# Optimization experiments

Hardware: AMD Instinct MI355X
Metric: run time of the kernel (lower is better)

## Reference

```python
import jax, jax.numpy as jnp
import numpy as np

EMBED_DIM = 768
N_HEADS = 12
HEAD_DIM = EMBED_DIM // N_HEADS


def setup_inputs() -> dict:
    key = jax.random.key(0)
    ks = jax.random.split(key, 6)
    bsz, seq = 2, 4096
    hidden_states = jax.random.normal(ks[0], (bsz, seq, EMBED_DIM), dtype=jnp.float32)
    attention_mask = jnp.zeros((bsz, 1, 1, seq), dtype=jnp.float32)
    s = 1.0 / np.sqrt(EMBED_DIM)
    Wq = jax.random.normal(ks[1], (EMBED_DIM, EMBED_DIM), dtype=jnp.float32) * s
    Wk = jax.random.normal(ks[2], (EMBED_DIM, EMBED_DIM), dtype=jnp.float32) * s
    Wv = jax.random.normal(ks[3], (EMBED_DIM, EMBED_DIM), dtype=jnp.float32) * s
    Wo = jax.random.normal(ks[4], (EMBED_DIM, EMBED_DIM), dtype=jnp.float32) * s
    bo = jax.random.normal(ks[5], (EMBED_DIM,), dtype=jnp.float32) * s
    return {"hidden_states": hidden_states, "attention_mask": attention_mask,
            "Wq": Wq, "Wk": Wk, "Wv": Wv, "Wo": Wo, "bo": bo}


def reference(hidden_states, attention_mask, Wq, Wk, Wv, Wo, bo):
    bsz, seq, _ = hidden_states.shape
    scale = 1.0 / np.sqrt(HEAD_DIM)

    def split_heads(x):  # [b, s, e] -> [b, h, s, d]
        return x.reshape(bsz, seq, N_HEADS, HEAD_DIM).transpose(0, 2, 1, 3)

    # nn.Linear applies x @ W.T
    q = split_heads(hidden_states @ Wq.T)
    k = split_heads(hidden_states @ Wk.T)
    v = split_heads(hidden_states @ Wv.T)

    # [b, h, tgt, src] score matrix (faithful to the bmm+softmax+bmm original)
    attn = jnp.einsum('bhqd,bhkd->bhqk', q, k) * scale
    attn = attn + attention_mask  # mask broadcasts [b,1,1,src]
    probs = jax.nn.softmax(attn, axis=-1)
    ctx = jnp.einsum('bhqk,bhkd->bhqd', probs, v)

    concat = ctx.transpose(0, 2, 1, 3).reshape(bsz, seq, EMBED_DIM)
    return concat @ Wo.T + bo
```

## Files before the change

kernel.cpp:

```cpp
#include <hip/hip_runtime.h>
#include <stdint.h>

#define ED   768
#define NH   12
#define HD   64
#define SEQ  4096
#define BSZ  2
#define BHT  (BSZ*NH)
#define MTOT (BSZ*SEQ)

typedef short bf16x8  __attribute__((ext_vector_type(8)));
typedef float f32x4   __attribute__((ext_vector_type(4)));
typedef float f32x16  __attribute__((ext_vector_type(16)));

#define LOG2E 1.44269504088896340736f
#define C2    (0.125f * LOG2E)

__device__ __forceinline__ unsigned short f2bf(float f) {
    union { float f; uint32_t u; } v; v.f = f;
    uint32_t u = v.u;
    u += 0x7fffu + ((u >> 16) & 1u);
    return (unsigned short)(u >> 16);
}

__device__ __forceinline__ void cp16(const unsigned short* g, unsigned short* l) {
    __builtin_amdgcn_global_load_lds(
        (const __attribute__((address_space(1))) unsigned int*)(const void*)g,
        (__attribute__((address_space(3))) unsigned int*)(void*)l,
        16, 0, 0);
}

#define H_CHUNKS  (MTOT * ED / 4)
#define W_CHUNKS  (ED * ED / 4)
#define CVT_TOTAL (H_CHUNKS + 4 * W_CHUNKS)

__global__ __launch_bounds__(256) void convert_bf16(
    const float* __restrict__ H,  const float* __restrict__ Wq,
    const float* __restrict__ Wk, const float* __restrict__ Wv,
    const float* __restrict__ Wo, unsigned short* __restrict__ dst,
    unsigned short* __restrict__ WoB) {
    int i4 = blockIdx.x * 256 + threadIdx.x;
    float4 v;
    ushort4* optr;
    if (i4 < H_CHUNKS) { v = ((const float4*)H)[i4]; optr = (ushort4*)dst + i4; }
    else {
        int j = i4 - H_CHUNKS;
        if (j < 3 * W_CHUNKS) {
            if (j < W_CHUNKS)          v = ((const float4*)Wq)[j];
            else if (j < 2 * W_CHUNKS) v = ((const float4*)Wk)[j - W_CHUNKS];
            else                       v = ((const float4*)Wv)[j - 2 * W_CHUNKS];
            optr = (ushort4*)dst + i4;
        } else {
            v = ((const float4*)Wo)[j - 3 * W_CHUNKS];
            optr = (ushort4*)WoB + (j - 3 * W_CHUNKS);
        }
    }
    ushort4 o;
    o.x = f2bf(v.x); o.y = f2bf(v.y); o.z = f2bf(v.z); o.w = f2bf(v.w);
    *optr = o;
}

__global__ __launch_bounds__(256) void qkv_gemm(
    const unsigned short* __restrict__ Hb,
    const unsigned short* __restrict__ Wb,
    unsigned short* __restrict__ qkv) {
    __shared__ __align__(16) unsigned short Ah[128 * 64];
    __shared__ __align__(16) unsigned short Bh[128 * 64];
    const int t = threadIdx.x, w = t >> 6, lane = t & 63;
    const int quad = lane >> 4, r16 = lane & 15;
    const int wm = w >> 1, wn = w & 1;
    const int m0 = blockIdx.y * 128, n0g = blockIdx.x * 128;
    const int wsel = n0g / ED, n0 = n0g % ED;
    const int lrow = lane >> 3;
    const int lchs = ((lane & 7) ^ (lrow & 7)) * 8;

    f32x4 acc[4][4] = {};
    for (int kt = 0; kt < ED / 64; ++kt) {
        const int k0 = kt * 64;
#pragma unroll
        for (int i = 0; i < 4; ++i) {
            int row = i * 32 + w * 8;
            cp16(&Hb[(size_t)(m0 + row + lrow) * ED + k0 + lchs], &Ah[row * 64]);
            cp16(&Wb[(size_t)(n0g + row + lrow) * ED + k0 + lchs], &Bh[row * 64]);
        }
        __syncthreads();
#pragma unroll
        for (int kk = 0; kk < 2; ++kk) {
            bf16x8 aF[4], bF[4];
#pragma unroll
            for (int mi = 0; mi < 4; ++mi) {
                int R = wm * 64 + mi * 16 + r16;
                aF[mi] = *(const bf16x8*)&Ah[R * 64 + (((kk * 4 + quad) ^ (r16 & 7)) * 8)];
            }
#pragma unroll
            for (int ni = 0; ni < 4; ++ni) {
                int R = wn * 64 + ni * 16 + r16;
                bF[ni] = *(const bf16x8*)&Bh[R * 64 + (((kk * 4 + quad) ^ (r16 & 7)) * 8)];
            }
            if (wsel == 2) {
#pragma unroll
                for (int mi = 0; mi < 4; ++mi)
#pragma unroll
                    for (int ni = 0; ni < 4; ++ni)
                        acc[mi][ni] = __builtin_amdgcn_mfma_f32_16x16x32_bf16(
                            bF[ni], aF[mi], acc[mi][ni], 0, 0, 0);
            } else {
#pragma unroll
                for (int mi = 0; mi < 4; ++mi)
#pragma unroll
                    for (int ni = 0; ni < 4; ++ni)
                        acc[mi][ni] = __builtin_amdgcn_mfma_f32_16x16x32_bf16(
                            aF[mi], bF[ni], acc[mi][ni], 0, 0, 0);
            }
        }
        __syncthreads();
    }
    const size_t WSZ = (size_t)BHT * SEQ * HD;
    if (wsel == 2) {
#pragma unroll
        for (int mi = 0; mi < 4; ++mi)
#pragma unroll
            for (int ni = 0; ni < 4; ++ni)
#pragma unroll
                for (int r = 0; r < 4; ++r) {
                    int m  = m0 + wm * 64 + mi * 16 + r16;
                    int nn = n0 + wn * 64 + ni * 16 + quad * 4 + r;
                    int b = m >> 12, s = m & 4095;
                    int hh = nn >> 6, dd = nn & 63;
                    qkv[2 * WSZ + (((size_t)b * NH + hh) * HD + dd) * SEQ + s] =
                        f2bf(acc[mi][ni][r]);
                }
    } else {
        const float sc = (wsel == 0) ? C2 : 1.0f;
#pragma unroll
        for (int mi = 0; mi < 4; ++mi)
#pragma unroll
            for (int ni = 0; ni < 4; ++ni)
#pragma unroll
                for (int r = 0; r < 4; ++r) {
                    int m = m0 + wm * 64 + mi * 16 + quad * 4 + r;
                    int b = m >> 12, s = m & 4095;
                    int nn = n0 + wn * 64 + ni * 16 + r16;
                    int hh = nn >> 6, dd = nn & 63;
                    size_t off = (((size_t)b * NH + hh) * SEQ + s) * HD + dd;
                    qkv[(size_t)wsel * WSZ + off] = f2bf(acc[mi][ni][r] * sc);
                }
    }
}

__global__ __launch_bounds__(256) void flash_attn(
    const unsigned short* __restrict__ qkv, const float* __restrict__ mask,
    unsigned short* __restrict__ ctx) {
    __shared__ __align__(16) unsigned short Ksm[64 * 64];
    __shared__ __align__(16) unsigned short Vtsm[64 * 64];
    __shared__ __align__(16) unsigned short Psm[4][32][72];
    __shared__ unsigned short Msm[64];
    const int t  = threadIdx.x;
    const int bh = blockIdx.y;
    const int b  = bh / NH;
    const int h  = bh % NH;
    const int qbase = blockIdx.x * 128;
    const size_t WSZ = (size_t)BHT * SEQ * HD;
    const unsigned short* Qp = qkv + (size_t)bh * SEQ * HD;
    const unsigned short* Kp = Qp + WSZ;
    const unsigned short* Vt = qkv + 2 * WSZ + (size_t)bh * HD * SEQ;
    const int w = t >> 6, lane = t & 63, n31 = lane & 31, hi = lane >> 5;
    const int lrow = lane >> 3;
    const int lchs = ((lane & 7) ^ (lrow & 7)) * 8;

    bf16x8 qF[4];
    {
        int qrow = qbase + w * 32 + n31;
#pragma unroll
        for (int kc = 0; kc < 4; ++kc)
            qF[kc] = *(const bf16x8*)&Qp[(size_t)qrow * HD + kc * 16 + hi * 8];
    }
    bf16x8 bOnes = {};
    if (hi == 0) bOnes[0] = (short)0x3F80;

    f32x16 oAcc[2] = {};
    float l_i = 0.0f;
    const int sw = n31 & 7;

    for (int kt = 0; kt < SEQ / 64; ++kt) {
#pragma unroll
        for (int i = 0; i < 2; ++i) {
            int row = w * 16 + i * 8;
            cp16(&Kp[(size_t)(kt * 64 + row + lrow) * HD + lchs], &Ksm[row * 64]);
            cp16(&Vt[(size_t)(row + lrow) * SEQ + kt * 64 + lchs], &Vtsm[row * 64]);
        }
        if (t < 64) Msm[t] = f2bf(LOG2E * mask[b * SEQ + kt * 64 + t]);
        __syncthreads();

        float p[2][16];
        float rs0 = 0.f, rs1 = 0.f, rs2 = 0.f, rs3 = 0.f;
#pragma unroll
        for (int st = 0; st < 2; ++st) {
            bf16x8 am = {};
            {
                unsigned short mv = Msm[st * 32 + n31];
                am[0] = (hi == 0) ? (short)mv : (short)0;
            }
            f32x16 sA = {};
            sA = __builtin_amdgcn_mfma_f32_32x32x16_bf16(am, bOnes, sA, 0, 0, 0);
#pragma unroll
            for (int kc = 0; kc < 4; ++kc) {
                bf16x8 kF = *(const bf16x8*)
                    &Ksm[(st * 32 + n31) * 64 + (((2 * kc + hi) ^ sw) * 8)];
                sA = __builtin_amdgcn_mfma_f32_32x32x16_bf16(kF, qF[kc], sA, 0, 0, 0);
            }
#pragma unroll
            for (int r = 0; r < 16; ++r) p[st][r] = __builtin_amdgcn_exp2f(sA[r]);
            rs0 += p[st][0] + p[st][4] + p[st][8]  + p[st][12];
            rs1 += p[st][1] + p[st][5] + p[st][9]  + p[st][13];
            rs2 += p[st][2] + p[st][6] + p[st][10] + p[st][14];
            rs3 += p[st][3] + p[st][7] + p[st][11] + p[st][15];
        }
        l_i += (rs0 + rs1) + (rs2 + rs3);

#pragma unroll
        for (int st = 0; st < 2; ++st)
#pragma unroll
            for (int g = 0; g < 4; ++g) {
                union { float f; uint32_t u; } a0, a1, a2, a3;
                a0.f = p[st][4 * g + 0]; a1.f = p[st][4 * g + 1];
                a2.f = p[st][4 * g + 2]; a3.f = p[st][4 * g + 3];
                uint32_t d0 = __builtin_amdgcn_perm(a1.u + 0x8000u, a0.u + 0x8000u, 0x07060302u);
                uint32_t d1 = __builtin_amdgcn_perm(a3.u + 0x8000u, a2.u + 0x8000u, 0x07060302u);
                uint2 dd; dd.x = d0; dd.y = d1;
                *(uint2*)&Psm[w][n31][st * 32 + hi * 4 + 8 * g] = dd;
            }

#pragma unroll
        for (int kc = 0; kc < 4; ++kc) {
            bf16x8 pF = *(const bf16x8*)&Psm[w][n31][kc * 16 + hi * 8];
#pragma unroll
            for (int dt = 0; dt < 2; ++dt) {
                bf16x8 vF = *(const bf16x8*)
                    &Vtsm[(dt * 32 + n31) * 64 + (((2 * kc + hi) ^ sw) * 8)];
                oAcc[dt] = __builtin_amdgcn_mfma_f32_32x32x16_bf16(vF, pF, oAcc[dt], 0, 0, 0);
            }
        }
        __syncthreads();
    }
    l_i += __shfl_xor(l_i, 32);
    float inv = 1.0f / l_i;
    int s = qbase + w * 32 + n31;
    unsigned short* obase = &ctx[((size_t)b * SEQ + s) * ED + h * HD];
#pragma unroll
    for (int dt = 0; dt < 2; ++dt)
#pragma unroll
        for (int g = 0; g < 4; ++g) {
            ushort4 o;
            o.x = f2bf(oAcc[dt][4 * g + 0] * inv);
            o.y = f2bf(oAcc[dt][4 * g + 1] * inv);
            o.z = f2bf(oAcc[dt][4 * g + 2] * inv);
            o.w = f2bf(oAcc[dt][4 * g + 3] * inv);
            *(ushort4*)&obase[dt * 32 + hi * 4 + 8 * g] = o;
        }
}

__global__ __launch_bounds__(256) void out_gemm(
    const unsigned short* __restrict__ Ab,
    const unsigned short* __restrict__ Wob,
    const float* __restrict__ bo, float* __restrict__ out) {
    __shared__ __align__(16) unsigned short Ah[128 * 64];
    __shared__ __align__(16) unsigned short Bh[128 * 64];
    const int t = threadIdx.x, w = t >> 6, lane = t & 63;
    const int quad = lane >> 4, r16 = lane & 15;
    const int wm = w >> 1, wn = w & 1;
    const int m0 = blockIdx.y * 128, n0 = blockIdx.x * 128;
    const int lrow = lane >> 3;
    const int lchs = ((lane & 7) ^ (lrow & 7)) * 8;

    f32x4 acc[4][4] = {};
    for (int kt = 0; kt < ED / 64; ++kt) {
        const int k0 = kt * 64;
#pragma unroll
        for (int i = 0; i < 4; ++i) {
            int row = i * 32 + w * 8;
            cp16(&Ab[(size_t)(m0 + row + lrow) * ED + k0 + lchs], &Ah[row * 64]);
            cp16(&Wob[(size_t)(n0 + row + lrow) * ED + k0 + lchs], &Bh[row * 64]);
        }
        __syncthreads();
#pragma unroll
        for (int kk = 0; kk < 2; ++kk) {
            bf16x8 aF[4], bF[4];
#pragma unroll
            for (int mi = 0; mi < 4; ++mi) {
                int R = wm * 64 + mi * 16 + r16;
                aF[mi] = *(const bf16x8*)&Ah[R * 64 + (((kk * 4 + quad) ^ (r16 & 7)) * 8)];
            }
#pragma unroll
            for (int ni = 0; ni < 4; ++ni) {
                int R = wn * 64 + ni * 16 + r16;
                bF[ni] = *(const bf16x8*)&Bh[R * 64 + (((kk * 4 + quad) ^ (r16 & 7)) * 8)];
            }
#pragma unroll
            for (int mi = 0; mi < 4; ++mi)
#pragma unroll
                for (int ni = 0; ni < 4; ++ni)
                    acc[mi][ni] = __builtin_amdgcn_mfma_f32_16x16x32_bf16(
                        aF[mi], bF[ni], acc[mi][ni], 0, 0, 0);
        }
        __syncthreads();
    }
    float bov[4];
#pragma unroll
    for (int ni = 0; ni < 4; ++ni) bov[ni] = bo[n0 + wn * 64 + ni * 16 + r16];
#pragma unroll
    for (int mi = 0; mi < 4; ++mi)
#pragma unroll
        for (int ni = 0; ni < 4; ++ni)
#pragma unroll
            for (int r = 0; r < 4; ++r) {
                int m = m0 + wm * 64 + mi * 16 + quad * 4 + r;
                int n = n0 + wn * 64 + ni * 16 + r16;
                out[(size_t)m * ED + n] = acc[mi][ni][r] + bov[ni];
            }
}

extern "C" void kernel_launch(void* const* d_in, const int* in_sizes, int n_in,
                              void* d_out, int out_size, void* d_ws, size_t ws_size,
                              hipStream_t stream) {
    const float* H    = (const float*)d_in[0];
    const float* mask = (const float*)d_in[1];
    const float* Wq   = (const float*)d_in[2];
    const float* Wk   = (const float*)d_in[3];
    const float* Wv   = (const float*)d_in[4];
    const float* Wo   = (const float*)d_in[5];
    const float* bo   = (const float*)d_in[6];
    unsigned short* ws = (unsigned short*)d_ws;
    const size_t WSZ = (size_t)BHT * SEQ * HD;
    unsigned short* qkv = ws;
    unsigned short* ctx = ws + 3 * WSZ;
    unsigned short* WoB = ctx + (size_t)MTOT * ED;
    float* out = (float*)d_out;
    unsigned short* Hb = (unsigned short*)d_out;
    unsigned short* Wb = Hb + (size_t)MTOT * ED;

    convert_bf16<<<CVT_TOTAL / 256, 256, 0, stream>>>(H, Wq, Wk, Wv, Wo, Hb, WoB);
    qkv_gemm<<<dim3(3 * ED / 128, MTOT / 128), 256, 0, stream>>>(Hb, Wb, qkv);
    flash_attn<<<dim3(SEQ / 128, BHT), 256, 0, stream>>>(qkv, mask, ctx);
    out_gemm<<<dim3(ED / 128, MTOT / 128), 256, 0, stream>>>(ctx, WoB, bo, out);
}
```

Measured before the change: 306.9 us.

## Split KV range across wave pairs with two query fragments per wave

Restructures flash attention so each wave handles 64 query rows (two 32-row fragments) and the four waves form two pairs that each process alternating 64-key tiles. Each K fragment loaded from LDS is now reused for two query fragments, and each iteration covers 128 keys, halving the number of block barriers. The partial outputs and row sums of the two halves are combined through shared memory at the end. In exchange, shared memory use and accumulator register pressure roughly double, and the kernel gains an extra combine step.

```diff
diff --git a/kernel.cpp b/kernel.cpp
--- a/kernel.cpp
+++ b/kernel.cpp
@@ -151,10 +151,10 @@
 __global__ __launch_bounds__(256) void flash_attn(
     const unsigned short* __restrict__ qkv, const float* __restrict__ mask,
     unsigned short* __restrict__ ctx) {
-    __shared__ __align__(16) unsigned short Ksm[64 * 64];
-    __shared__ __align__(16) unsigned short Vtsm[64 * 64];
-    __shared__ __align__(16) unsigned short Psm[4][32][72];
-    __shared__ unsigned short Msm[64];
+    __shared__ __align__(16) unsigned short KVbuf[4][64 * 64];
+    __shared__ __align__(16) unsigned short Psm[4][64][72];
+    __shared__ unsigned short Msm[128];
+    __shared__ float lComb[2][2][32];
     const int t  = threadIdx.x;
     const int bh = blockIdx.y;
     const int b  = bh / NH;
@@ -165,99 +165,149 @@
     const unsigned short* Kp = Qp + WSZ;
     const unsigned short* Vt = qkv + 2 * WSZ + (size_t)bh * HD * SEQ;
     const int w = t >> 6, lane = t & 63, n31 = lane & 31, hi = lane >> 5;
+    const int par = w >> 1, qh = w & 1;
     const int lrow = lane >> 3;
     const int lchs = ((lane & 7) ^ (lrow & 7)) * 8;
-
-    bf16x8 qF[4];
-    {
-        int qrow = qbase + w * 32 + n31;
+    const int sw = n31 & 7;
+
+    bf16x8 qF[2][4];
+#pragma unroll
+    for (int qf = 0; qf < 2; ++qf) {
+        int qrow = qbase + qh * 64 + qf * 32 + n31;
 #pragma unroll
         for (int kc = 0; kc < 4; ++kc)
-            qF[kc] = *(const bf16x8*)&Qp[(size_t)qrow * HD + kc * 16 + hi * 8];
+            qF[qf][kc] = *(const bf16x8*)&Qp[(size_t)qrow * HD + kc * 16 + hi * 8];
     }
     bf16x8 bOnes = {};
     if (hi == 0) bOnes[0] = (short)0x3F80;
-
-    f32x16 oAcc[2] = {};
-    float l_i = 0.0f;
-    const int sw = n31 & 7;
-
-    for (int kt = 0; kt < SEQ / 64; ++kt) {
-#pragma unroll
-        for (int i = 0; i < 2; ++i) {
-            int row = w * 16 + i * 8;
-            cp16(&Kp[(size_t)(kt * 64 + row + lrow) * HD + lchs], &Ksm[row * 64]);
-            cp16(&Vt[(size_t)(row + lrow) * SEQ + kt * 64 + lchs], &Vtsm[row * 64]);
-        }
-        if (t < 64) Msm[t] = f2bf(LOG2E * mask[b * SEQ + kt * 64 + t]);
-        __syncthreads();
-
-        float p[2][16];
-        float rs0 = 0.f, rs1 = 0.f, rs2 = 0.f, rs3 = 0.f;
+    const f32x16 kZero = {};
+
+    f32x16 oAcc[2][2] = {};
+    float l_[2] = {0.0f, 0.0f};
+
+    for (int r = 0; r < SEQ / 128; ++r) {
+        {
+            unsigned short* dst = KVbuf[w];
+            int ktile = 2 * r + qh;
+            if (w < 2) {
+#pragma unroll
+                for (int i = 0; i < 8; ++i)
+                    cp16(&Kp[(size_t)(ktile * 64 + i * 8 + lrow) * HD + lchs],
+                         &dst[i * 8 * 64]);
+            } else {
+#pragma unroll
+                for (int i = 0; i < 8; ++i)
+                    cp16(&Vt[(size_t)(i * 8 + lrow) * SEQ + ktile * 64 + lchs],
+                         &dst[i * 8 * 64]);
+            }
+        }
+        if (t < 128) Msm[t] = f2bf(LOG2E * mask[b * SEQ + r * 128 + t]);
+        __syncthreads();
+
+        const unsigned short* Ks = KVbuf[par];
+        const unsigned short* Vs = KVbuf[2 + par];
+
 #pragma unroll
         for (int st = 0; st < 2; ++st) {
             bf16x8 am = {};
             {
-                unsigned short mv = Msm[st * 32 + n31];
+                unsigned short mv = Msm[par * 64 + st * 32 + n31];
                 am[0] = (hi == 0) ? (short)mv : (short)0;
             }
-            f32x16 sA = {};
-            sA = __builtin_amdgcn_mfma_f32_32x32x16_bf16(am, bOnes, sA, 0, 0, 0);
+            f32x16 sM = __builtin_amdgcn_mfma_f32_32x32x16_bf16(am, bOnes, kZero, 0, 0, 0);
+            bf16x8 kF[4];
+#pragma unroll
+            for (int kc = 0; kc < 4; ++kc)
+                kF[kc] = *(const bf16x8*)
+                    &Ks[(st * 32 + n31) * 64 + (((2 * kc + hi) ^ sw) * 8)];
+            f32x16 sA0 = sM, sA1 = sM;
 #pragma unroll
             for (int kc = 0; kc < 4; ++kc) {
-                bf16x8 kF = *(const bf16x8*)
-                    &Ksm[(st * 32 + n31) * 64 + (((2 * kc + hi) ^ sw) * 8)];
-                sA = __builtin_amdgcn_mfma_f32_32x32x16_bf16(kF, qF[kc], sA, 0, 0, 0);
-            }
-#pragma unroll
-            for (int r = 0; r < 16; ++r) p[st][r] = __builtin_amdgcn_exp2f(sA[r]);
-            rs0 += p[st][0] + p[st][4] + p[st][8]  + p[st][12];
-            rs1 += p[st][1] + p[st][5] + p[st][9]  + p[st][13];
-            rs2 += p[st][2] + p[st][6] + p[st][10] + p[st][14];
-            rs3 += p[st][3] + p[st][7] + p[st][11] + p[st][15];
-        }
-        l_i += (rs0 + rs1) + (rs2 + rs3);
-
-#pragma unroll
-        for (int st = 0; st < 2; ++st)
-#pragma unroll
-            for (int g = 0; g < 4; ++g) {
-                union { float f; uint32_t u; } a0, a1, a2, a3;
-                a0.f = p[st][4 * g + 0]; a1.f = p[st][4 * g + 1];
-                a2.f = p[st][4 * g + 2]; a3.f = p[st][4 * g + 3];
-                uint32_t d0 = __builtin_amdgcn_perm(a1.u + 0x8000u, a0.u + 0x8000u, 0x07060302u);
-                uint32_t d1 = __builtin_amdgcn_perm(a3.u + 0x8000u, a2.u + 0x8000u, 0x07060302u);
-                uint2 dd; dd.x = d0; dd.y = d1;
-                *(uint2*)&Psm[w][n31][st * 32 + hi * 4 + 8 * g] = dd;
-            }
+                sA0 = __builtin_amdgcn_mfma_f32_32x32x16_bf16(kF[kc], qF[0][kc], sA0, 0, 0, 0);
+                sA1 = __builtin_amdgcn_mfma_f32_32x32x16_bf16(kF[kc], qF[1][kc], sA1, 0, 0, 0);
+            }
+#pragma unroll
+            for (int qf = 0; qf < 2; ++qf) {
+                const f32x16& sA = qf ? sA1 : sA0;
+                float p[16];
+                float r0 = 0.f, r1 = 0.f, r2 = 0.f, r3 = 0.f;
+#pragma unroll
+                for (int g = 0; g < 4; ++g) {
+                    p[4 * g + 0] = __builtin_amdgcn_exp2f(sA[4 * g + 0]);
+                    p[4 * g + 1] = __builtin_amdgcn_exp2f(sA[4 * g + 1]);
+                    p[4 * g + 2] = __builtin_amdgcn_exp2f(sA[4 * g + 2]);
+                    p[4 * g + 3] = __builtin_amdgcn_exp2f(sA[4 * g + 3]);
+                    r0 += p[4 * g + 0]; r1 += p[4 * g + 1];
+                    r2 += p[4 * g + 2]; r3 += p[4 * g + 3];
+                }
+                l_[qf] += (r0 + r1) + (r2 + r3);
+#pragma unroll
+                for (int g = 0; g < 4; ++g) {
+                    union { float f; uint32_t u; } a0, a1, a2, a3;
+                    a0.f = p[4 * g + 0]; a1.f = p[4 * g + 1];
+                    a2.f = p[4 * g + 2]; a3.f = p[4 * g + 3];
+                    uint32_t d0 = __builtin_amdgcn_perm(a1.u + 0x8000u, a0.u + 0x8000u, 0x07060302u);
+                    uint32_t d1 = __builtin_amdgcn_perm(a3.u + 0x8000u, a2.u + 0x8000u, 0x07060302u);
+                    uint2 dd; dd.x = d0; dd.y = d1;
+                    *(uint2*)&Psm[w][qf * 32 + n31][st * 32 + hi * 4 + 8 * g] = dd;
+                }
+            }
+        }
 
 #pragma unroll
         for (int kc = 0; kc < 4; ++kc) {
-            bf16x8 pF = *(const bf16x8*)&Psm[w][n31][kc * 16 + hi * 8];
+            bf16x8 pF0 = *(const bf16x8*)&Psm[w][n31][kc * 16 + hi * 8];
+            bf16x8 pF1 = *(const bf16x8*)&Psm[w][32 + n31][kc * 16 + hi * 8];
 #pragma unroll
             for (int dt = 0; dt < 2; ++dt) {
                 bf16x8 vF = *(const bf16x8*)
-                    &Vtsm[(dt * 32 + n31) * 64 + (((2 * kc + hi) ^ sw) * 8)];
-                oAcc[dt] = __builtin_amdgcn_mfma_f32_32x32x16_bf16(vF, pF, oAcc[dt], 0, 0, 0);
-            }
-        }
-        __syncthreads();
-    }
-    l_i += __shfl_xor(l_i, 32);
-    float inv = 1.0f / l_i;
-    int s = qbase + w * 32 + n31;
-    unsigned short* obase = &ctx[((size_t)b * SEQ + s) * ED + h * HD];
-#pragma unroll
-    for (int dt = 0; dt < 2; ++dt)
-#pragma unroll
-        for (int g = 0; g < 4; ++g) {
-            ushort4 o;
-            o.x = f2bf(oAcc[dt][4 * g + 0] * inv);
-            o.y = f2bf(oAcc[dt][4 * g + 1] * inv);
-            o.z = f2bf(oAcc[dt][4 * g + 2] * inv);
-            o.w = f2bf(oAcc[dt][4 * g + 3] * inv);
-            *(ushort4*)&obase[dt * 32 + hi * 4 + 8 * g] = o;
-        }
+                    &Vs[(dt * 32 + n31) * 64 + (((2 * kc + hi) ^ sw) * 8)];
+                oAcc[0][dt] = __builtin_amdgcn_mfma_f32_32x32x16_bf16(vF, pF0, oAcc[0][dt], 0, 0, 0);
+                oAcc[1][dt] = __builtin_amdgcn_mfma_f32_32x32x16_bf16(vF, pF1, oAcc[1][dt], 0, 0, 0);
+            }
+        }
+        __syncthreads();
+    }
+
+    l_[0] += __shfl_xor(l_[0], 32);
+    l_[1] += __shfl_xor(l_[1], 32);
+    float* comb = (float*)KVbuf;
+    if (par == 1) {
+#pragma unroll
+        for (int qf = 0; qf < 2; ++qf)
+#pragma unroll
+            for (int dt = 0; dt < 2; ++dt)
+#pragma unroll
+                for (int g = 0; g < 4; ++g) {
+                    float4 v;
+                    v.x = oAcc[qf][dt][4 * g + 0]; v.y = oAcc[qf][dt][4 * g + 1];
+                    v.z = oAcc[qf][dt][4 * g + 2]; v.w = oAcc[qf][dt][4 * g + 3];
+                    *(float4*)&comb[qh * 4096 + lane * 64 + (qf * 2 + dt) * 16 + 4 * g] = v;
+                }
+        if (hi == 0) { lComb[qh][0][n31] = l_[0]; lComb[qh][1][n31] = l_[1]; }
+    }
+    __syncthreads();
+    if (par == 0) {
+#pragma unroll
+        for (int qf = 0; qf < 2; ++qf) {
+            float inv = 1.0f / (l_[qf] + lComb[qh][qf][n31]);
+            int s = qbase + qh * 64 + qf * 32 + n31;
+            unsigned short* obase = &ctx[((size_t)b * SEQ + s) * ED + h * HD];
+#pragma unroll
+            for (int dt = 0; dt < 2; ++dt)
+#pragma unroll
+                for (int g = 0; g < 4; ++g) {
+                    float4 v = *(const float4*)
+                        &comb[qh * 4096 + lane * 64 + (qf * 2 + dt) * 16 + 4 * g];
+                    ushort4 o;
+                    o.x = f2bf((oAcc[qf][dt][4 * g + 0] + v.x) * inv);
+                    o.y = f2bf((oAcc[qf][dt][4 * g + 1] + v.y) * inv);
+                    o.z = f2bf((oAcc[qf][dt][4 * g + 2] + v.z) * inv);
+                    o.w = f2bf((oAcc[qf][dt][4 * g + 3] + v.w) * inv);
+                    *(ushort4*)&obase[dt * 32 + hi * 4 + 8 * g] = o;
+                }
+        }
+    }
 }
 
 __global__ __launch_bounds__(256) void out_gemm(
```

Result: slower. 314.7 us (+2.5%).
